# Kernel optimization log

Hardware: AMD Instinct MI355X
Metric: run time of the kernel (lower is better)

## Reference

```python
import jax, jax.numpy as jnp
import numpy as np

B, S, D = 1, 2048, 4096
H, KV, HD = 32, 8, 128
C = 4096  # cache length
THETA = 1000000.0
NEG = -1e9


def setup_inputs() -> dict:
    key = jax.random.key(0)
    ks = jax.random.split(key, 8)
    std = 0.02
    x = jax.random.normal(ks[0], (B, S, D), jnp.float32)
    wq = jax.random.normal(ks[1], (H * HD, D), jnp.float32) * std
    wk = jax.random.normal(ks[2], (KV * HD, D), jnp.float32) * std
    wv = jax.random.normal(ks[3], (KV * HD, D), jnp.float32) * std
    wo = jax.random.normal(ks[4], (D, H * HD), jnp.float32) * std
    k_cache = jnp.zeros((B, KV, C, HD), jnp.float32)
    v_cache = jnp.zeros((B, KV, C, HD), jnp.float32)
    # rotary tables (real/imag of freqs_cis)
    inv_freq = 1.0 / (THETA ** (jnp.arange(0, HD, 2, dtype=jnp.float32) / HD))  # [HD/2]
    t = jnp.arange(C, dtype=jnp.float32)
    freqs = jnp.outer(t, inv_freq)  # [C, HD/2]
    cos, sin = jnp.cos(freqs), jnp.sin(freqs)
    # causal additive mask over cache positions
    mask = jnp.where(jnp.tril(jnp.ones((C, C), bool)), 0.0, NEG).astype(jnp.float32)
    storage_idx = jnp.arange(S, dtype=jnp.int32)
    return {"x": x, "wq": wq, "wk": wk, "wv": wv, "wo": wo,
            "k_cache": k_cache, "v_cache": v_cache,
            "cos": cos, "sin": sin, "mask": mask, "storage_idx": storage_idx}


def _rope(x, cos, sin):
    # x: [B, h, S, HD]; cos/sin: [S, HD/2] -> complex mult on interleaved pairs
    xr, xi = x[..., 0::2], x[..., 1::2]
    c = cos[None, None, :, :]
    s = sin[None, None, :, :]
    or_, oi_ = xr * c - xi * s, xr * s + xi * c
    return jnp.stack([or_, oi_], axis=-1).reshape(x.shape)


def reference(x, wq, wk, wv, wo, k_cache, v_cache, cos, sin, mask, storage_idx):
    bsz, seqlen, _ = x.shape
    xq = jnp.einsum('bsd,ed->bse', x, wq).reshape(bsz, seqlen, H, HD).transpose(0, 2, 1, 3)
    xk = jnp.einsum('bsd,ed->bse', x, wk).reshape(bsz, seqlen, KV, HD).transpose(0, 2, 1, 3)
    xv = jnp.einsum('bsd,ed->bse', x, wv).reshape(bsz, seqlen, KV, HD).transpose(0, 2, 1, 3)
    cos_g, sin_g = cos[storage_idx], sin[storage_idx]
    xq = _rope(xq, cos_g, sin_g)
    xk = _rope(xk, cos_g, sin_g)
    # scatter into KV cache at storage_idx along the position axis
    keys = k_cache.at[:, :, storage_idx, :].set(xk)
    values = v_cache.at[:, :, storage_idx, :].set(xv)
    # GQA: repeat kv heads (kv-head-major, matches expand+reshape)
    rep = H // KV
    keys = jnp.repeat(keys, rep, axis=1)      # [B, H, C, HD]
    values = jnp.repeat(values, rep, axis=1)  # [B, H, C, HD]
    scores = jnp.einsum('bhqd,bhkd->bhqk', xq, keys) / np.sqrt(HD)
    scores = scores + mask[storage_idx][None, None, :, :]
    attn = jax.nn.softmax(scores, axis=-1)
    out = jnp.einsum('bhqk,bhkd->bhqd', attn, values)
    out = out.transpose(0, 2, 1, 3).reshape(bsz, seqlen, H * HD)
    return jnp.einsum('bse,de->bsd', out, wo)
```

## Files before the change

kernel.cpp:

```cpp
#include <hip/hip_runtime.h>
#include <cstdint>
#include <cstddef>

#define S_LEN 2048
#define DM    4096
#define NH    32
#define NKV   8
#define HDIM  128
#define EQ    4096
#define EKV   1024
#define SCALE 0.08838834764831845f
#define SC_LOG2E 0.1275325477889277f

typedef unsigned short u16;
typedef short bf16x8 __attribute__((ext_vector_type(8)));
typedef float f32x4  __attribute__((ext_vector_type(4)));

__device__ __forceinline__ u16 f2bf(float f) {
  union { float f; unsigned u; } v; v.f = f;
  unsigned r = v.u + 0x7FFFu + ((v.u >> 16) & 1u);
  return (u16)(r >> 16);
}
__device__ __forceinline__ float bf2f(u16 b) {
  union { unsigned u; float f; } v; v.u = ((unsigned)b) << 16;
  return v.f;
}
__device__ __forceinline__ void glds16(const void* g, void* l) {
  __builtin_amdgcn_global_load_lds((const __attribute__((address_space(1))) void*)g,
                                   (__attribute__((address_space(3))) void*)l, 16, 0, 0);
}

__global__ void cast_all(const float* __restrict__ x, const float* __restrict__ wq,
                         const float* __restrict__ wk, const float* __restrict__ wv,
                         const float* __restrict__ wo,
                         u16* __restrict__ xb, u16* __restrict__ wqb,
                         u16* __restrict__ wkb, u16* __restrict__ wvb,
                         u16* __restrict__ wob) {
  const size_t stride = (size_t)gridDim.x * blockDim.x;
  for (size_t u = (size_t)blockIdx.x * blockDim.x + threadIdx.x; u < 12582912u; u += stride) {
    const float* in; u16* outp; size_t i;
    if (u < 2097152u)      { in = x;  outp = xb;  i = u; }
    else if (u < 6291456u) { in = wq; outp = wqb; i = u - 2097152u; }
    else if (u < 7340032u) { in = wk; outp = wkb; i = u - 6291456u; }
    else if (u < 8388608u) { in = wv; outp = wvb; i = u - 7340032u; }
    else                   { in = wo; outp = wob; i = u - 8388608u; }
    float4 f = ((const float4*)in)[i];
    ushort4 b;
    b.x = f2bf(f.x); b.y = f2bf(f.y); b.z = f2bf(f.z); b.w = f2bf(f.w);
    ((ushort4*)outp)[i] = b;
  }
}

__device__ __forceinline__ void stage_half(const u16* __restrict__ g, int ldg, int k0,
                                           u16* ldsp, int t) {
  const int wb = t & ~63;
#pragma unroll
  for (int j = 0; j < 2; ++j) {
    const int U = j * 512 + t;
    const int row = U >> 3, u = U & 7;
    const int uu = u ^ (row & 7);
    glds16(g + (size_t)row * ldg + k0 + uu * 8, ldsp + (size_t)(j * 512 + wb) * 8);
  }
}

#define LOADA(MH) \
  { _Pragma("unroll") for (int m_ = 0; m_ < 4; ++m_) { \
      _Pragma("unroll") for (int kk_ = 0; kk_ < 2; ++kk_) { \
        afr[MH][m_][kk_] = *(const bf16x8*)&lds[aRd + arow + ((MH)*64 + m_*16)*64 + axo[kk_]]; } } }

#define LOADB(NH) \
  { _Pragma("unroll") for (int n_ = 0; n_ < 2; ++n_) { \
      _Pragma("unroll") for (int kk_ = 0; kk_ < 2; ++kk_) { \
        bfr[n_][kk_] = *(const bf16x8*)&lds[bRd + brow + ((NH)*32 + n_*16)*64 + axo[kk_]]; } } }

#define MFMA16(MH, NH) \
  { _Pragma("unroll") for (int m_ = 0; m_ < 4; ++m_) \
    _Pragma("unroll") for (int n_ = 0; n_ < 2; ++n_) \
    _Pragma("unroll") for (int kk_ = 0; kk_ < 2; ++kk_) \
      acc[(MH)*4+m_][(NH)*2+n_] = __builtin_amdgcn_mfma_f32_16x16x32_bf16( \
        afr[MH][m_][kk_], bfr[n_][kk_], acc[(MH)*4+m_][(NH)*2+n_], 0, 0, 0); }

#define GBAR() __builtin_amdgcn_s_barrier()
#define WLG()  { asm volatile("s_waitcnt lgkmcnt(0)" ::: "memory"); __builtin_amdgcn_sched_barrier(0); }
#define WVM4() { asm volatile("s_waitcnt vmcnt(4)" ::: "memory"); __builtin_amdgcn_sched_barrier(0); }

template<bool QKV3>
__global__ __launch_bounds__(512, 2)
void gemm8(const u16* __restrict__ A, const u16* __restrict__ B,
           void* __restrict__ Cq, u16* __restrict__ Ck, u16* __restrict__ Cv,
           int K) {
  __shared__ u16 lds[65536];
  const int t = threadIdx.x;
  const int l = t & 63, lr = l & 15, lg = l >> 4;
  const int wid = t >> 6, wm = wid >> 2, wn = wid & 3;
  const int m0 = blockIdx.y * 256, n0 = blockIdx.x * 256;
  const int KT = K >> 6;

  const int arow = lr * 64;
  const int brow = ((wn & 1) * 64 + lr) * 64;
  int axo[2];
  axo[0] = (lg ^ (lr & 7)) * 8;
  axo[1] = ((4 + lg) ^ (lr & 7)) * 8;

  const u16* Alo = A + (size_t)m0 * K;
  const u16* Ahi = A + (size_t)(m0 + 128) * K;
  const u16* Blo = B + (size_t)n0 * K;
  const u16* Bhi = B + (size_t)(n0 + 128) * K;

  f32x4 acc[8][4] = {};
  bf16x8 afr[2][4][2], bfr[2][2];

  stage_half(Blo, K, 0, &lds[32768], t);
  stage_half(Bhi, K, 0, &lds[32768 + 8192], t);
  stage_half(Alo, K, 0, &lds[0], t);
  stage_half(Ahi, K, 0, &lds[8192], t);
  stage_half(Alo, K, 64, &lds[16384], t);
  stage_half(Ahi, K, 64, &lds[24576], t);
  asm volatile("s_waitcnt vmcnt(0)" ::: "memory");
  GBAR();

#pragma unroll 1
  for (int tau = 0; tau < KT; ++tau) {
    const int P = tau & 1;
    const int aRd = (P * 2 + wm) * 8192;
    const int bRd = 32768 + (P * 2 + (wn >> 1)) * 8192;
    const int bSt = 32768 + (1 - P) * 16384;
    const int aSt = P * 16384;
    const int kB = (tau + 1 < KT ? tau + 1 : KT - 1) * 64;
    const int kA = (tau + 2 < KT ? tau + 2 : KT - 1) * 64;

    LOADA(0) LOADB(0)
    stage_half(Blo, K, kB, &lds[bSt], t);
    GBAR(); WLG();
    __builtin_amdgcn_s_setprio(1); MFMA16(0, 0); __builtin_amdgcn_s_setprio(0);
    GBAR();
    LOADA(1)
    stage_half(Bhi, K, kB, &lds[bSt + 8192], t);
    GBAR(); WLG();
    __builtin_amdgcn_s_setprio(1); MFMA16(1, 0); __builtin_amdgcn_s_setprio(0);
    GBAR();
    LOADB(1)
    stage_half(Alo, K, kA, &lds[aSt], t);
    GBAR(); WLG();
    __builtin_amdgcn_s_setprio(1); MFMA16(0, 1); __builtin_amdgcn_s_setprio(0);
    GBAR();
    stage_half(Ahi, K, kA, &lds[aSt + 8192], t);
    GBAR(); WVM4();
    __builtin_amdgcn_s_setprio(1); MFMA16(1, 1); __builtin_amdgcn_s_setprio(0);
    GBAR();
  }

#pragma unroll
  for (int am = 0; am < 8; ++am) {
    const int row = m0 + wm * 128 + (am >> 2) * 64 + (am & 3) * 16 + lg * 4;
#pragma unroll
    for (int an = 0; an < 4; ++an) {
      const int col = wn * 64 + (an >> 1) * 32 + (an & 1) * 16 + lr;
#pragma unroll
      for (int r = 0; r < 4; ++r) {
        if constexpr (QKV3) {
          u16* cp; int ldc, cc;
          if (n0 < 4096)      { cp = (u16*)Cq; ldc = 4096; cc = n0 + col; }
          else if (n0 < 5120) { cp = Ck;       ldc = 1024; cc = n0 - 4096 + col; }
          else                { cp = Cv;       ldc = 1024; cc = n0 - 5120 + col; }
          cp[(size_t)(row + r) * ldc + cc] = f2bf(acc[am][an][r]);
        } else {
          ((float*)Cq)[(size_t)(row + r) * 4096 + n0 + col] = acc[am][an][r];
        }
      }
    }
  }
}

__global__ void rope_all(u16* __restrict__ qd, u16* __restrict__ kd,
                         const float* __restrict__ cosb, const float* __restrict__ sinb,
                         const int* __restrict__ sidx) {
  const int u = blockIdx.x * blockDim.x + threadIdx.x;
  u16* base; int s, b;
  if (u < 1048576) {
    base = qd + (size_t)u * 8;
    s = u >> 9;
    b = u & 15;
  } else if (u < 1310720) {
    const int u2 = u - 1048576;
    base = kd + (size_t)u2 * 8;
    s = u2 >> 7;
    b = u2 & 15;
  } else return;
  const int pos = sidx[s];
  const float4 c  = *(const float4*)&cosb[pos * 64 + b * 4];
  const float4 sn = *(const float4*)&sinb[pos * 64 + b * 4];
  uint4 raw = *(uint4*)base;
  u16* pe = (u16*)&raw;
  const float cc[4] = {c.x, c.y, c.z, c.w};
  const float ss[4] = {sn.x, sn.y, sn.z, sn.w};
#pragma unroll
  for (int j = 0; j < 4; ++j) {
    const float xr = bf2f(pe[2 * j]), xi = bf2f(pe[2 * j + 1]);
    pe[2 * j]     = f2bf(xr * cc[j] - xi * ss[j]);
    pe[2 * j + 1] = f2bf(xr * ss[j] + xi * cc[j]);
  }
  *(uint4*)base = raw;
}

__global__ void transpose_v(const u16* __restrict__ v, u16* __restrict__ vt) {
  __shared__ u16 tile[32][33];
  const int tx = threadIdx.x, ty = threadIdx.y;
  const int c0 = blockIdx.x * 32, s0 = blockIdx.y * 32;
#pragma unroll
  for (int j = 0; j < 32; j += 8)
    tile[ty + j][tx] = v[(size_t)(s0 + ty + j) * EKV + c0 + tx];
  __syncthreads();
#pragma unroll
  for (int j = 0; j < 32; j += 8)
    vt[(size_t)(c0 + ty + j) * S_LEN + s0 + tx] = tile[tx][ty + j];
}

__global__ __launch_bounds__(256, 2)
void attn_fwd(const u16* __restrict__ q, const u16* __restrict__ k,
              const u16* __restrict__ vt, u16* __restrict__ ao) {
  __shared__ u16 lK[64 * 128];
  __shared__ u16 lV[128 * 64];
  __shared__ u16 lP[4 * 16 * 72];
  const int t = threadIdx.x, w = t >> 6, l = t & 63;
  const int lr = l & 15, lg = l >> 4;
  const int wb = t & ~63;
  const int p = blockIdx.x, h = blockIdx.y;
  const int kvh = h >> 2;
  u16* lPw = &lP[w * (16 * 72)];

#pragma unroll 1
  for (int ph = 0; ph < 2; ++ph) {
    const int qt = ph ? (31 - p) : p;
    const int q0 = qt * 64 + w * 16;
    const int nt = qt + 1;

    bf16x8 qa[4];
#pragma unroll
    for (int kc = 0; kc < 4; ++kc)
      qa[kc] = *(const bf16x8*)&q[(size_t)(q0 + lr) * EQ + h * HDIM + kc * 32 + lg * 8];

    f32x4 o[8] = {};
    float mrun[4], lrun[4];
#pragma unroll
    for (int r = 0; r < 4; ++r) { mrun[r] = -1e30f; lrun[r] = 0.f; }

    for (int tk = 0; tk < nt; ++tk) {
      const int kv0 = tk * 64;
      __syncthreads();
#pragma unroll
      for (int hh = 0; hh < 4; ++hh) {
        const int f = hh * 256 + t;
        { const int row = f >> 4, u = f & 15, us = u ^ (row & 7);
          glds16(&k[(size_t)(kv0 + row) * EKV + kvh * HDIM + us * 8], &lK[(hh * 256 + wb) * 8]); }
        { const int row = f >> 3, u = f & 7, us = u ^ (row & 7);
          glds16(&vt[(size_t)(kvh * HDIM + row) * S_LEN + kv0 + us * 8], &lV[(hh * 256 + wb) * 8]); }
      }
      __syncthreads();

      f32x4 sc[4] = {};
#pragma unroll
      for (int n = 0; n < 4; ++n) {
#pragma unroll
        for (int kc = 0; kc < 4; ++kc) {
          const int row = n * 16 + lr;
          const int us = (kc * 4 + lg) ^ (row & 7);
          bf16x8 bk = *(const bf16x8*)&lK[row * 128 + us * 8];
          sc[n] = __builtin_amdgcn_mfma_f32_16x16x32_bf16(qa[kc], bk, sc[n], 0, 0, 0);
        }
      }

#pragma unroll
      for (int n = 0; n < 4; ++n) {
        const int kvc = kv0 + n * 16 + lr;
#pragma unroll
        for (int r = 0; r < 4; ++r) {
          const int qr = q0 + lg * 4 + r;
          const float v = sc[n][r] * SC_LOG2E;
          sc[n][r] = (kvc > qr) ? -1e30f : v;
        }
      }
#pragma unroll
      for (int r = 0; r < 4; ++r) {
        float v = fmaxf(fmaxf(sc[0][r], sc[1][r]), fmaxf(sc[2][r], sc[3][r]));
        v = fmaxf(v, __shfl_xor(v, 1));
        v = fmaxf(v, __shfl_xor(v, 2));
        v = fmaxf(v, __shfl_xor(v, 4));
        v = fmaxf(v, __shfl_xor(v, 8));
        const float mn = fmaxf(mrun[r], v);
        const float sf = __builtin_amdgcn_exp2f(mrun[r] - mn);
        mrun[r] = mn;
        float rs = 0.f;
#pragma unroll
        for (int n = 0; n < 4; ++n) {
          const float pv = __builtin_amdgcn_exp2f(sc[n][r] - mn);
          sc[n][r] = pv;
          rs += pv;
        }
        rs += __shfl_xor(rs, 1);
        rs += __shfl_xor(rs, 2);
        rs += __shfl_xor(rs, 4);
        rs += __shfl_xor(rs, 8);
        lrun[r] = lrun[r] * sf + rs;
#pragma unroll
        for (int nh = 0; nh < 8; ++nh) o[nh][r] *= sf;
      }
#pragma unroll
      for (int n = 0; n < 4; ++n)
#pragma unroll
        for (int r = 0; r < 4; ++r)
          lPw[(lg * 4 + r) * 72 + n * 16 + lr] = f2bf(sc[n][r]);

#pragma unroll
      for (int kc2 = 0; kc2 < 2; ++kc2) {
        bf16x8 pa = *(const bf16x8*)&lPw[lr * 72 + kc2 * 32 + lg * 8];
#pragma unroll
        for (int nh = 0; nh < 8; ++nh) {
          const int row = nh * 16 + lr;
          const int us = (kc2 * 4 + lg) ^ (row & 7);
          bf16x8 bv = *(const bf16x8*)&lV[row * 64 + us * 8];
          o[nh] = __builtin_amdgcn_mfma_f32_16x16x32_bf16(pa, bv, o[nh], 0, 0, 0);
        }
      }
    }

#pragma unroll
    for (int nh = 0; nh < 8; ++nh)
#pragma unroll
      for (int r = 0; r < 4; ++r) {
        const float val = o[nh][r] / lrun[r];
        ao[(size_t)(q0 + lg * 4 + r) * EQ + h * HDIM + nh * 16 + lr] = f2bf(val);
      }
  }
}

extern "C" void kernel_launch(void* const* d_in, const int* in_sizes, int n_in,
                              void* d_out, int out_size, void* d_ws, size_t ws_size,
                              hipStream_t stream) {
  (void)in_sizes; (void)n_in; (void)out_size; (void)ws_size;
  const float* x    = (const float*)d_in[0];
  const float* wq   = (const float*)d_in[1];
  const float* wk   = (const float*)d_in[2];
  const float* wv   = (const float*)d_in[3];
  const float* wo   = (const float*)d_in[4];
  const float* cosb = (const float*)d_in[7];
  const float* sinb = (const float*)d_in[8];
  const int*   sidx = (const int*)d_in[10];
  float* out = (float*)d_out;

  u16* ws  = (u16*)d_ws;
  u16* xb  = ws;
  u16* wqb = xb  + (size_t)S_LEN * DM;
  u16* wkb = wqb + (size_t)EQ * DM;
  u16* wvb = wkb + (size_t)EKV * DM;
  u16* wob = wvb + (size_t)EKV * DM;
  u16* qb  = wob + (size_t)DM * EQ;
  u16* kb  = qb  + (size_t)S_LEN * EQ;
  u16* vb  = kb  + (size_t)S_LEN * EKV;
  u16* vtb = vb  + (size_t)S_LEN * EKV;
  u16* aob = vtb + (size_t)S_LEN * EKV;

  cast_all<<<2048, 256, 0, stream>>>(x, wq, wk, wv, wo, xb, wqb, wkb, wvb, wob);
  gemm8<true><<<dim3(24, 8), 512, 0, stream>>>(xb, wqb, qb, kb, vb, DM);
  rope_all<<<5120, 256, 0, stream>>>(qb, kb, cosb, sinb, sidx);
  transpose_v<<<dim3(EKV / 32, S_LEN / 32), dim3(32, 8), 0, stream>>>(vb, vtb);
  attn_fwd<<<dim3(16, NH), 256, 0, stream>>>(qb, kb, vtb, aob);
  gemm8<false><<<dim3(16, 8), 512, 0, stream>>>(aob, wob, out, nullptr, nullptr, EQ);
}
```

Baseline: 366.0 us.

## Shrink GEMM N-tile so both projection grids fill every compute unit

Result: faster. 326.0 us (-10.9%).

```diff
diff --git a/kernel.cpp b/kernel.cpp
--- a/kernel.cpp
+++ b/kernel.cpp
@@ -51,53 +51,55 @@
   }
 }
 
-__device__ __forceinline__ void stage_half(const u16* __restrict__ g, int ldg, int k0,
-                                           u16* ldsp, int t) {
+template<int UN>
+__device__ __forceinline__ void stage_units(const u16* __restrict__ g, int ldg, int k0,
+                                            u16* ldsp, int t) {
   const int wb = t & ~63;
 #pragma unroll
-  for (int j = 0; j < 2; ++j) {
+  for (int j = 0; j * 512 < UN; ++j) {
     const int U = j * 512 + t;
-    const int row = U >> 3, u = U & 7;
-    const int uu = u ^ (row & 7);
-    glds16(g + (size_t)row * ldg + k0 + uu * 8, ldsp + (size_t)(j * 512 + wb) * 8);
-  }
-}
-
-#define LOADA(MH) \
+    if ((UN % 512 == 0) || (U < UN)) {
+      const int row = U >> 3, u = U & 7;
+      const int uu = u ^ (row & 7);
+      glds16(g + (size_t)row * ldg + k0 + uu * 8, ldsp + (size_t)(j * 512 + wb) * 8);
+    }
+  }
+}
+
+#define LOADA2(MH) \
   { _Pragma("unroll") for (int m_ = 0; m_ < 4; ++m_) { \
       _Pragma("unroll") for (int kk_ = 0; kk_ < 2; ++kk_) { \
         afr[MH][m_][kk_] = *(const bf16x8*)&lds[aRd + arow + ((MH)*64 + m_*16)*64 + axo[kk_]]; } } }
 
-#define LOADB(NH) \
-  { _Pragma("unroll") for (int n_ = 0; n_ < 2; ++n_) { \
-      _Pragma("unroll") for (int kk_ = 0; kk_ < 2; ++kk_) { \
-        bfr[n_][kk_] = *(const bf16x8*)&lds[bRd + brow + ((NH)*32 + n_*16)*64 + axo[kk_]]; } } }
-
-#define MFMA16(MH, NH) \
+#define LOADBK(KK) \
+  { _Pragma("unroll") for (int n_ = 0; n_ < NF; ++n_) { \
+        bfr[KK][n_] = *(const bf16x8*)&lds[bRd + ((wn & 1)*16*NF + n_*16 + lr)*64 + axo[KK]]; } }
+
+#define MFMAC(MH, KK) \
   { _Pragma("unroll") for (int m_ = 0; m_ < 4; ++m_) \
-    _Pragma("unroll") for (int n_ = 0; n_ < 2; ++n_) \
-    _Pragma("unroll") for (int kk_ = 0; kk_ < 2; ++kk_) \
-      acc[(MH)*4+m_][(NH)*2+n_] = __builtin_amdgcn_mfma_f32_16x16x32_bf16( \
-        afr[MH][m_][kk_], bfr[n_][kk_], acc[(MH)*4+m_][(NH)*2+n_], 0, 0, 0); }
+    _Pragma("unroll") for (int n_ = 0; n_ < NF; ++n_) \
+      acc[(MH)*4+m_][n_] = __builtin_amdgcn_mfma_f32_16x16x32_bf16( \
+        afr[MH][m_][KK], bfr[KK][n_], acc[(MH)*4+m_][n_], 0, 0, 0); }
 
 #define GBAR() __builtin_amdgcn_s_barrier()
 #define WLG()  { asm volatile("s_waitcnt lgkmcnt(0)" ::: "memory"); __builtin_amdgcn_sched_barrier(0); }
 #define WVM4() { asm volatile("s_waitcnt vmcnt(4)" ::: "memory"); __builtin_amdgcn_sched_barrier(0); }
 
-template<bool QKV3>
+template<int NF, bool QKV3>
 __global__ __launch_bounds__(512, 2)
 void gemm8(const u16* __restrict__ A, const u16* __restrict__ B,
            void* __restrict__ Cq, u16* __restrict__ Ck, u16* __restrict__ Cv,
            int K) {
-  __shared__ u16 lds[65536];
+  constexpr int BSLOT = 2048 * NF;
+  constexpr int BUN   = 256 * NF;
+  __shared__ u16 lds[32768 + 4 * BSLOT];
   const int t = threadIdx.x;
   const int l = t & 63, lr = l & 15, lg = l >> 4;
   const int wid = t >> 6, wm = wid >> 2, wn = wid & 3;
-  const int m0 = blockIdx.y * 256, n0 = blockIdx.x * 256;
+  const int m0 = blockIdx.y * 256, n0 = blockIdx.x * (64 * NF);
   const int KT = K >> 6;
 
   const int arow = lr * 64;
-  const int brow = ((wn & 1) * 64 + lr) * 64;
   int axo[2];
   axo[0] = (lg ^ (lr & 7)) * 8;
   axo[1] = ((4 + lg) ^ (lr & 7)) * 8;
@@ -105,17 +107,17 @@
   const u16* Alo = A + (size_t)m0 * K;
   const u16* Ahi = A + (size_t)(m0 + 128) * K;
   const u16* Blo = B + (size_t)n0 * K;
-  const u16* Bhi = B + (size_t)(n0 + 128) * K;
-
-  f32x4 acc[8][4] = {};
-  bf16x8 afr[2][4][2], bfr[2][2];
-
-  stage_half(Blo, K, 0, &lds[32768], t);
-  stage_half(Bhi, K, 0, &lds[32768 + 8192], t);
-  stage_half(Alo, K, 0, &lds[0], t);
-  stage_half(Ahi, K, 0, &lds[8192], t);
-  stage_half(Alo, K, 64, &lds[16384], t);
-  stage_half(Ahi, K, 64, &lds[24576], t);
+  const u16* Bhi = B + (size_t)(n0 + 32 * NF) * K;
+
+  f32x4 acc[8][NF] = {};
+  bf16x8 afr[2][4][2], bfr[2][NF];
+
+  stage_units<BUN>(Blo, K, 0, &lds[32768], t);
+  stage_units<BUN>(Bhi, K, 0, &lds[32768 + BSLOT], t);
+  stage_units<1024>(Alo, K, 0, &lds[0], t);
+  stage_units<1024>(Ahi, K, 0, &lds[8192], t);
+  stage_units<1024>(Alo, K, 64, &lds[16384], t);
+  stage_units<1024>(Ahi, K, 64, &lds[24576], t);
   asm volatile("s_waitcnt vmcnt(0)" ::: "memory");
   GBAR();
 
@@ -123,30 +125,29 @@
   for (int tau = 0; tau < KT; ++tau) {
     const int P = tau & 1;
     const int aRd = (P * 2 + wm) * 8192;
-    const int bRd = 32768 + (P * 2 + (wn >> 1)) * 8192;
-    const int bSt = 32768 + (1 - P) * 16384;
+    const int bRd = 32768 + (P * 2 + (wn >> 1)) * BSLOT;
+    const int bSt = 32768 + (1 - P) * 2 * BSLOT;
     const int aSt = P * 16384;
     const int kB = (tau + 1 < KT ? tau + 1 : KT - 1) * 64;
     const int kA = (tau + 2 < KT ? tau + 2 : KT - 1) * 64;
 
-    LOADA(0) LOADB(0)
-    stage_half(Blo, K, kB, &lds[bSt], t);
+    LOADA2(0) LOADBK(0)
+    stage_units<BUN>(Blo, K, kB, &lds[bSt], t);
     GBAR(); WLG();
-    __builtin_amdgcn_s_setprio(1); MFMA16(0, 0); __builtin_amdgcn_s_setprio(0);
-    GBAR();
-    LOADA(1)
-    stage_half(Bhi, K, kB, &lds[bSt + 8192], t);
+    __builtin_amdgcn_s_setprio(1); MFMAC(0, 0); __builtin_amdgcn_s_setprio(0);
+    GBAR();
+    LOADA2(1) LOADBK(1)
+    stage_units<BUN>(Bhi, K, kB, &lds[bSt + BSLOT], t);
     GBAR(); WLG();
-    __builtin_amdgcn_s_setprio(1); MFMA16(1, 0); __builtin_amdgcn_s_setprio(0);
-    GBAR();
-    LOADB(1)
-    stage_half(Alo, K, kA, &lds[aSt], t);
-    GBAR(); WLG();
-    __builtin_amdgcn_s_setprio(1); MFMA16(0, 1); __builtin_amdgcn_s_setprio(0);
-    GBAR();
-    stage_half(Ahi, K, kA, &lds[aSt + 8192], t);
+    __builtin_amdgcn_s_setprio(1); MFMAC(1, 0); __builtin_amdgcn_s_setprio(0);
+    GBAR();
+    stage_units<1024>(Alo, K, kA, &lds[aSt], t);
+    GBAR();
+    __builtin_amdgcn_s_setprio(1); MFMAC(0, 1); __builtin_amdgcn_s_setprio(0);
+    GBAR();
+    stage_units<1024>(Ahi, K, kA, &lds[aSt + 8192], t);
     GBAR(); WVM4();
-    __builtin_amdgcn_s_setprio(1); MFMA16(1, 1); __builtin_amdgcn_s_setprio(0);
+    __builtin_amdgcn_s_setprio(1); MFMAC(1, 1); __builtin_amdgcn_s_setprio(0);
     GBAR();
   }
 
@@ -154,18 +155,19 @@
   for (int am = 0; am < 8; ++am) {
     const int row = m0 + wm * 128 + (am >> 2) * 64 + (am & 3) * 16 + lg * 4;
 #pragma unroll
-    for (int an = 0; an < 4; ++an) {
-      const int col = wn * 64 + (an >> 1) * 32 + (an & 1) * 16 + lr;
+    for (int an = 0; an < NF; ++an) {
+      const int gc = n0 + wn * (16 * NF) + an * 16 + lr;
 #pragma unroll
       for (int r = 0; r < 4; ++r) {
         if constexpr (QKV3) {
-          u16* cp; int ldc, cc;
-          if (n0 < 4096)      { cp = (u16*)Cq; ldc = 4096; cc = n0 + col; }
-          else if (n0 < 5120) { cp = Ck;       ldc = 1024; cc = n0 - 4096 + col; }
-          else                { cp = Cv;       ldc = 1024; cc = n0 - 5120 + col; }
-          cp[(size_t)(row + r) * ldc + cc] = f2bf(acc[am][an][r]);
+          if (gc < 4096)
+            ((u16*)Cq)[(size_t)(row + r) * 4096 + gc] = f2bf(acc[am][an][r]);
+          else if (gc < 5120)
+            Ck[(size_t)(row + r) * 1024 + (gc - 4096)] = f2bf(acc[am][an][r]);
+          else
+            Cv[(size_t)(row + r) * 1024 + (gc - 5120)] = f2bf(acc[am][an][r]);
         } else {
-          ((float*)Cq)[(size_t)(row + r) * 4096 + n0 + col] = acc[am][an][r];
+          ((float*)Cq)[(size_t)(row + r) * 4096 + gc] = acc[am][an][r];
         }
       }
     }
@@ -361,9 +363,9 @@
   u16* aob = vtb + (size_t)S_LEN * EKV;
 
   cast_all<<<2048, 256, 0, stream>>>(x, wq, wk, wv, wo, xb, wqb, wkb, wvb, wob);
-  gemm8<true><<<dim3(24, 8), 512, 0, stream>>>(xb, wqb, qb, kb, vb, DM);
+  gemm8<3, true><<<dim3(32, 8), 512, 0, stream>>>(xb, wqb, qb, kb, vb, DM);
   rope_all<<<5120, 256, 0, stream>>>(qb, kb, cosb, sinb, sidx);
   transpose_v<<<dim3(EKV / 32, S_LEN / 32), dim3(32, 8), 0, stream>>>(vb, vtb);
   attn_fwd<<<dim3(16, NH), 256, 0, stream>>>(qb, kb, vtb, aob);
-  gemm8<false><<<dim3(16, 8), 512, 0, stream>>>(aob, wob, out, nullptr, nullptr, EQ);
-}
+  gemm8<2, false><<<dim3(32, 8), 512, 0, stream>>>(aob, wob, out, nullptr, nullptr, EQ);
+}
```
